# Kernel optimization log

Hardware: AMD Instinct MI355X
Metric: run time of the kernel (lower is better)

## Reference

```python
import jax, jax.numpy as jnp
import numpy as np

T, HID, H, HKV, D = 4096, 2048, 16, 2, 128
EPS = 1e-6


def setup_inputs() -> dict:
    key = jax.random.key(0)
    ks = jax.random.split(key, 5)
    hidden_states = jax.random.normal(ks[0], (T, HID), dtype=jnp.float32)
    # rope angles: build realistic cos/sin from positions and inv-freqs
    inv_freq = 1.0 / (10000.0 ** (jnp.arange(0, D, 2, dtype=jnp.float32) / D))
    ang = jnp.arange(T, dtype=jnp.float32)[:, None] * inv_freq[None, :]  # [T, D/2]
    ang = jnp.concatenate([ang, ang], axis=-1)  # [T, D]
    cos, sin = jnp.cos(ang), jnp.sin(ang)
    w_qkv = jax.random.normal(ks[1], (HID, (2 * H + 2 * HKV) * D), dtype=jnp.float32) * (HID ** -0.5)
    w_o = jax.random.normal(ks[2], (H * D, HID), dtype=jnp.float32) * ((H * D) ** -0.5)
    q_norm_w = jnp.ones((D,), dtype=jnp.float32)
    k_norm_w = jnp.ones((D,), dtype=jnp.float32)
    return {"hidden_states": hidden_states, "cos": cos, "sin": sin,
            "w_qkv": w_qkv, "w_o": w_o, "q_norm_w": q_norm_w, "k_norm_w": k_norm_w}


def _rms_norm(x, w):
    var = jnp.mean(x * x, axis=-1, keepdims=True)
    return x * jax.lax.rsqrt(var + EPS) * w


def _rotate_half(x):
    x1, x2 = x[..., : D // 2], x[..., D // 2:]
    return jnp.concatenate([-x2, x1], axis=-1)


def _rope(x, cos, sin):
    # x: [T, h, D]; cos/sin: [T, D]
    return x * cos[:, None, :] + _rotate_half(x) * sin[:, None, :]


def reference(hidden_states, cos, sin, w_qkv, w_o, q_norm_w, k_norm_w):
    qkv = hidden_states @ w_qkv  # [T, (2H+2HKV)*D]
    q_sz, kv_sz = 2 * H * D, HKV * D
    # packed query+gate: view as [T, H, 2D], first half query, second half gate
    qg = qkv[:, :q_sz].reshape(T, H, 2 * D)
    q, gate = qg[..., :D], qg[..., D:]
    k = qkv[:, q_sz:q_sz + kv_sz].reshape(T, HKV, D)
    v = qkv[:, q_sz + kv_sz:].reshape(T, HKV, D)
    q = _rms_norm(q, q_norm_w)
    k = _rms_norm(k, k_norm_w)
    q = _rope(q, cos, sin)
    k = _rope(k, cos, sin)
    # GQA: expand kv heads to H
    rep = H // HKV
    k = jnp.repeat(k, rep, axis=1)  # [T, H, D]
    v = jnp.repeat(v, rep, axis=1)
    scale = D ** -0.5
    scores = jnp.einsum('thd,shd->hts', q, k) * scale  # [H, T, T]
    causal = jnp.tril(jnp.ones((T, T), dtype=bool))
    scores = jnp.where(causal[None], scores, jnp.finfo(scores.dtype).min)
    probs = jax.nn.softmax(scores, axis=-1)
    attn = jnp.einsum('hts,shd->thd', probs, v)  # [T, H, D]
    out = attn.reshape(T, H * D) * jax.nn.sigmoid(gate.reshape(T, H * D))
    return out @ w_o
```

## Files before the change

kernel.cpp:

```cpp
#include <hip/hip_runtime.h>
#include <hip/hip_bf16.h>
#include <math.h>


namespace {
constexpr int kT   = 4096;
constexpr int kHid = 2048;
constexpr int kH   = 16;
constexpr int kHkv = 2;
constexpr int kD   = 128;
constexpr int kNqkv = (2 * kH + 2 * kHkv) * kD;
constexpr int kQsz  = 2 * kH * kD;
constexpr int kRowU = kNqkv * 2;
constexpr float kEps = 1e-6f;
constexpr float kScale = 0.08838834764831845f;
}

typedef __attribute__((ext_vector_type(8))) short short8;
typedef __attribute__((ext_vector_type(4))) float floatx4;

__device__ inline unsigned short f2bf(float x) {
  unsigned u = __float_as_uint(x);
  u = (u + 0x7fffu + ((u >> 16) & 1u)) >> 16;
  return (unsigned short)u;
}

__device__ inline void gload_lds16(const void* g, void* l) {
  typedef const __attribute__((address_space(1))) unsigned GQ;
  typedef __attribute__((address_space(3))) unsigned LQ;
  __builtin_amdgcn_global_load_lds((GQ*)g, (LQ*)l, 16, 0, 0);
}

__global__ __launch_bounds__(256)
void cvt_bf16(const float* __restrict__ in, unsigned short* __restrict__ out,
              long nelem) {
  long i = ((long)blockIdx.x * 256 + threadIdx.x) * 4;
  if (i >= nelem) return;
  float4 v = *(const float4*)(in + i);
  unsigned long long p = (unsigned long long)f2bf(v.x) |
                         ((unsigned long long)f2bf(v.y) << 16) |
                         ((unsigned long long)f2bf(v.z) << 32) |
                         ((unsigned long long)f2bf(v.w) << 48);
  *(unsigned long long*)(out + i) = p;
}

__global__ __launch_bounds__(256)
void transpose_cvt(const float* __restrict__ in, unsigned short* __restrict__ out,
                   int R, int C) {
  __shared__ float t[32][33];
  const int bx = blockIdx.x * 32;
  const int by = blockIdx.y * 32;
  const int x = threadIdx.x & 31, y = threadIdx.x >> 5;
#pragma unroll
  for (int j = 0; j < 4; ++j)
    t[y * 4 + j][x] = in[(long)(by + y * 4 + j) * C + bx + x];
  __syncthreads();
#pragma unroll
  for (int j = 0; j < 4; ++j)
    out[(long)(bx + y * 4 + j) * R + by + x] = f2bf(t[x][y * 4 + j]);
}

__global__ __launch_bounds__(256)
void vt_transpose(const float* __restrict__ qkv, unsigned short* __restrict__ VtG) {
  __shared__ float t[32][33];
  const int t0 = blockIdx.x * 32;
  const int c0 = blockIdx.y * 32;
  const int x = threadIdx.x & 31, y = threadIdx.x >> 5;
#pragma unroll
  for (int j = 0; j < 4; ++j)
    t[y * 4 + j][x] = qkv[(long)(t0 + y * 4 + j) * kNqkv + 4352 + c0 + x];
  __syncthreads();
#pragma unroll
  for (int j = 0; j < 4; ++j)
    VtG[(long)(c0 + y * 4 + j) * kT + t0 + x] = f2bf(t[x][y * 4 + j]);
}

__global__ __launch_bounds__(256)
void gemm_bf16(const unsigned short* __restrict__ A,
               const unsigned short* __restrict__ Bt, float* __restrict__ C,
               int M, int N, int K) {
  __shared__ __align__(16) unsigned short As[128 * 64];
  __shared__ __align__(16) unsigned short Bs[128 * 64];
  const int tid = threadIdx.x;
  const int lane = tid & 63;
  const int w = tid >> 6;
  const int wr = w >> 1, wc = w & 1;
  const int n = lane & 15;
  const int quad = lane >> 4;
  const long bm = (long)blockIdx.x * 128, bn = (long)blockIdx.y * 128;

  floatx4 acc[4][4];
  floatx4 zero = {0.f, 0.f, 0.f, 0.f};
#pragma unroll
  for (int a = 0; a < 4; ++a)
#pragma unroll
    for (int b = 0; b < 4; ++b) acc[a][b] = zero;

  for (int k0 = 0; k0 < K; k0 += 64) {
    __syncthreads();
#pragma unroll
    for (int it = 0; it < 4; ++it) {
      int ci = it * 256 + tid;
      int r = ci >> 3, c = ci & 7;
      int cg = c ^ (r & 7);
      gload_lds16(A + (bm + r) * (long)K + k0 + cg * 8, As + (it * 256 + w * 64) * 8);
      gload_lds16(Bt + (bn + r) * (long)K + k0 + cg * 8, Bs + (it * 256 + w * 64) * 8);
    }
    __syncthreads();

#pragma unroll
    for (int ks = 0; ks < 2; ++ks) {
      short8 af[4], bf[4];
#pragma unroll
      for (int a = 0; a < 4; ++a) {
        int m = wr * 64 + a * 16 + n;
        af[a] = *(const short8*)(As + m * 64 + ((4 * ks + quad) ^ (m & 7)) * 8);
      }
#pragma unroll
      for (int b = 0; b < 4; ++b) {
        int nn = wc * 64 + b * 16 + n;
        bf[b] = *(const short8*)(Bs + nn * 64 + ((4 * ks + quad) ^ (nn & 7)) * 8);
      }
#pragma unroll
      for (int a = 0; a < 4; ++a)
#pragma unroll
        for (int b = 0; b < 4; ++b)
          acc[a][b] = __builtin_amdgcn_mfma_f32_16x16x32_bf16(af[a], bf[b], acc[a][b], 0, 0, 0);
    }
  }
#pragma unroll
  for (int a = 0; a < 4; ++a)
#pragma unroll
    for (int b = 0; b < 4; ++b)
#pragma unroll
      for (int r = 0; r < 4; ++r)
        C[(bm + wr * 64 + a * 16 + quad * 4 + r) * (long)N + bn + wc * 64 + b * 16 + n] =
            acc[a][b][r];
}

__global__ __launch_bounds__(256)
void norm_rope_cvt(float* qkv, const float* __restrict__ cosb,
                   const float* __restrict__ sinb, const float* __restrict__ qw,
                   const float* __restrict__ kw) {
  unsigned short* qkvu = (unsigned short*)qkv;
  const int lane = threadIdx.x & 63;
  const int wslot = blockIdx.x * 4 + (threadIdx.x >> 6);
  const int nslots = gridDim.x * 4;
  for (int task = wslot; task < kT * 18; task += nslots) {
    const int t = task / 18;
    const int h = task % 18;
    const bool isq = (h < kH);
    const long base = (long)t * kNqkv + (isq ? h * 2 * kD : kQsz + (h - kH) * kD);
    float xlo = qkv[base + lane];
    float xhi = qkv[base + 64 + lane];
    float v = xlo * xlo + xhi * xhi;
#pragma unroll
    for (int off = 1; off < 64; off <<= 1) v += __shfl_xor(v, off, 64);
    float rms = rsqrtf(v * (1.0f / kD) + kEps);
    const float* wv = isq ? qw : kw;
    float nlo = xlo * rms * wv[lane];
    float nhi = xhi * rms * wv[64 + lane];
    float clo = cosb[t * kD + lane], chi = cosb[t * kD + 64 + lane];
    float slo = sinb[t * kD + lane], shi = sinb[t * kD + 64 + lane];
    float rlo = nlo * clo - nhi * slo;
    float rhi = nhi * chi + nlo * shi;
    if (isq) {
      float glo = qkv[base + kD + lane];
      float ghi = qkv[base + kD + 64 + lane];
      qkv[base + kD + lane] = 1.0f / (1.0f + __expf(-glo));
      qkv[base + kD + 64 + lane] = 1.0f / (1.0f + __expf(-ghi));
      qkvu[(long)t * kRowU + 512 * h + lane] = f2bf(rlo);
      qkvu[(long)t * kRowU + 512 * h + 64 + lane] = f2bf(rhi);
    } else {
      qkvu[(long)t * kRowU + 8192 + 256 * (h - kH) + lane] = f2bf(rlo);
      qkvu[(long)t * kRowU + 8192 + 256 * (h - kH) + 64 + lane] = f2bf(rhi);
    }
  }
}

__global__ __launch_bounds__(256)
void flash_attn_mfma(const unsigned short* qkvu, const float* qkvf,
                     const unsigned short* VtG, unsigned short* __restrict__ og) {
  __shared__ __align__(16) unsigned short Ks[64 * 128];
  __shared__ __align__(16) unsigned short Vt[128 * 64];
  __shared__ __align__(16) unsigned short Ps[128 * 64];

  const int tid = threadIdx.x;
  const int lane = tid & 63;
  const int w = tid >> 6;
  const int n = lane & 15;
  const int quad = lane >> 4;
  const int g = blockIdx.x;
  const int h = g & 15;
  const int bm = 31 - (g >> 4);
  const int hk = h >> 3;
  const int q0 = bm * 128;

  short8 qf[2][4];
#pragma unroll
  for (int mt = 0; mt < 2; ++mt) {
    const unsigned short* qrow =
        qkvu + (long)(q0 + 32 * w + 16 * mt + n) * kRowU + 512 * h;
#pragma unroll
    for (int ks = 0; ks < 4; ++ks)
      qf[mt][ks] = *(const short8*)(qrow + 32 * ks + 8 * quad);
  }
  short8 lfrag;
  {
    short o = (n == 0) ? (short)0x3F80 : (short)0;
    lfrag = (short8){o, o, o, o, o, o, o, o};
  }

  floatx4 O[2][8];
  floatx4 Ol[2];
  floatx4 zero = {0.f, 0.f, 0.f, 0.f};
#pragma unroll
  for (int mt = 0; mt < 2; ++mt) {
    Ol[mt] = zero;
#pragma unroll
    for (int dt = 0; dt < 8; ++dt) O[mt][dt] = zero;
  }

  const int kn_end = 2 * bm + 1;
  for (int kn = 0; kn <= kn_end; ++kn) {
    __syncthreads();
#pragma unroll
    for (int it = 0; it < 4; ++it) {
      int pc = (w * 4 + it) * 64 + lane;
      int r = pc >> 4, c = pc & 15;
      int lc = c ^ (r & 15);
      gload_lds16(qkvu + (long)(kn * 64 + r) * kRowU + 8192 + 256 * hk + 8 * lc,
                  Ks + (w * 4 + it) * 512);
    }
#pragma unroll
    for (int it = 0; it < 4; ++it) {
      int pc = (w * 4 + it) * 64 + lane;
      int d = pc >> 3, c = pc & 7;
      int lc = c ^ (d & 7);
      gload_lds16(VtG + (long)hk * (128 * kT) + (long)d * kT + kn * 64 + 8 * lc,
                  Vt + (w * 4 + it) * 512);
    }
    __syncthreads();

    floatx4 S[2][4];
#pragma unroll
    for (int mt = 0; mt < 2; ++mt)
#pragma unroll
      for (int ct = 0; ct < 4; ++ct) S[mt][ct] = zero;
#pragma unroll
    for (int ks = 0; ks < 4; ++ks) {
#pragma unroll
      for (int ct = 0; ct < 4; ++ct) {
        int row = 16 * ct + n;
        short8 kf = *(const short8*)(Ks + row * 128 + ((4 * ks + quad) ^ n) * 8);
        S[0][ct] = __builtin_amdgcn_mfma_f32_16x16x32_bf16(qf[0][ks], kf, S[0][ct], 0, 0, 0);
        S[1][ct] = __builtin_amdgcn_mfma_f32_16x16x32_bf16(qf[1][ks], kf, S[1][ct], 0, 0, 0);
      }
    }

    const bool needmask = (kn >= 2 * bm);
    const int jbase = (kn - 2 * bm) * 64;
    const int hi = n >> 3, lo = n & 7;
#pragma unroll
    for (int mt = 0; mt < 2; ++mt) {
#pragma unroll
      for (int r = 0; r < 4; ++r) {
        int prow = 32 * w + 16 * mt + quad * 4 + r;
        float p0 = __expf(S[mt][0][r] * kScale);
        float p1 = __expf(S[mt][1][r] * kScale);
        float p2 = __expf(S[mt][2][r] * kScale);
        float p3 = __expf(S[mt][3][r] * kScale);
        if (needmask) {
          if (jbase + n > prow) p0 = 0.f;
          if (jbase + 16 + n > prow) p1 = 0.f;
          if (jbase + 32 + n > prow) p2 = 0.f;
          if (jbase + 48 + n > prow) p3 = 0.f;
        }
        int sw = prow & 7;
        Ps[prow * 64 + (((0 + hi) ^ sw) << 3) + lo] = f2bf(p0);
        Ps[prow * 64 + (((2 + hi) ^ sw) << 3) + lo] = f2bf(p1);
        Ps[prow * 64 + (((4 + hi) ^ sw) << 3) + lo] = f2bf(p2);
        Ps[prow * 64 + (((6 + hi) ^ sw) << 3) + lo] = f2bf(p3);
      }
    }
    __asm__ volatile("s_waitcnt lgkmcnt(0)" ::: "memory");

#pragma unroll
    for (int ks = 0; ks < 2; ++ks) {
      int r0 = 32 * w + n, r1 = 32 * w + 16 + n;
      short8 pf0 = *(const short8*)(Ps + r0 * 64 + (((4 * ks + quad) ^ (r0 & 7)) << 3));
      short8 pf1 = *(const short8*)(Ps + r1 * 64 + (((4 * ks + quad) ^ (r1 & 7)) << 3));
      Ol[0] = __builtin_amdgcn_mfma_f32_16x16x32_bf16(pf0, lfrag, Ol[0], 0, 0, 0);
      Ol[1] = __builtin_amdgcn_mfma_f32_16x16x32_bf16(pf1, lfrag, Ol[1], 0, 0, 0);
#pragma unroll
      for (int dt = 0; dt < 8; ++dt) {
        int d = 16 * dt + n;
        short8 vf = *(const short8*)(Vt + d * 64 + (((4 * ks + quad) ^ (d & 7)) << 3));
        O[0][dt] = __builtin_amdgcn_mfma_f32_16x16x32_bf16(pf0, vf, O[0][dt], 0, 0, 0);
        O[1][dt] = __builtin_amdgcn_mfma_f32_16x16x32_bf16(pf1, vf, O[1][dt], 0, 0, 0);
      }
    }
  }

#pragma unroll
  for (int mt = 0; mt < 2; ++mt) {
#pragma unroll
    for (int r = 0; r < 4; ++r) {
      float l = __shfl(Ol[mt][r], quad << 4, 64);
      float inv = 1.0f / l;
      int row = q0 + 32 * w + 16 * mt + quad * 4 + r;
#pragma unroll
      for (int dt = 0; dt < 8; ++dt) {
        int col = 16 * dt + n;
        float gte = qkvf[(long)row * kNqkv + 256 * h + 128 + col];
        og[(long)row * kHid + 128 * h + col] = f2bf(O[mt][dt][r] * inv * gte);
      }
    }
  }
}

extern "C" void kernel_launch(void* const* d_in, const int* in_sizes, int n_in,
                              void* d_out, int out_size, void* d_ws, size_t ws_size,
                              hipStream_t stream) {
  (void)in_sizes; (void)n_in; (void)out_size; (void)ws_size;
  const float* hs   = (const float*)d_in[0];
  const float* cosb = (const float*)d_in[1];
  const float* sinb = (const float*)d_in[2];
  const float* wqkv = (const float*)d_in[3];
  const float* wo   = (const float*)d_in[4];
  const float* qw   = (const float*)d_in[5];
  const float* kw   = (const float*)d_in[6];
  float* out = (float*)d_out;

  char* ws = (char*)d_ws;
  float* qkv = (float*)ws;
  unsigned short* hsb = (unsigned short*)(ws + 75497472);
  unsigned short* og  = hsb;
  unsigned short* wt  = (unsigned short*)(ws + 92274688);
  unsigned short* VtG = wt;

  cvt_bf16<<<dim3(8192), 256, 0, stream>>>(hs, hsb, (long)kT * kHid);
  transpose_cvt<<<dim3(kNqkv / 32, kHid / 32), 256, 0, stream>>>(wqkv, wt, kHid, kNqkv);
  gemm_bf16<<<dim3(kT / 128, kNqkv / 128), 256, 0, stream>>>(hsb, wt, qkv, kT, kNqkv, kHid);
  vt_transpose<<<dim3(kT / 32, 8), 256, 0, stream>>>(qkv, VtG);
  norm_rope_cvt<<<dim3(2304), 256, 0, stream>>>(qkv, cosb, sinb, qw, kw);
  flash_attn_mfma<<<dim3(kT / 128 * kH), 256, 0, stream>>>((const unsigned short*)qkv, qkv, VtG, og);
  transpose_cvt<<<dim3(kHid / 32, kHid / 32), 256, 0, stream>>>(wo, wt, kHid, kHid);
  gemm_bf16<<<dim3(kT / 128, kHid / 128), 256, 0, stream>>>(og, wt, out, kT, kHid, kHid);
}
```

Baseline: 483.3 us.

## Split causal attention key range across two blocks and combine partials

```diff
diff --git a/kernel.cpp b/kernel.cpp
--- a/kernel.cpp
+++ b/kernel.cpp
@@ -23,6 +23,10 @@
   unsigned u = __float_as_uint(x);
   u = (u + 0x7fffu + ((u >> 16) & 1u)) >> 16;
   return (unsigned short)u;
+}
+
+__device__ inline float bf2f(unsigned short u) {
+  return __uint_as_float((unsigned)u << 16);
 }
 
 __device__ inline void gload_lds16(const void* g, void* l) {
@@ -179,8 +183,8 @@
 }
 
 __global__ __launch_bounds__(256)
-void flash_attn_mfma(const unsigned short* qkvu, const float* qkvf,
-                     const unsigned short* VtG, unsigned short* __restrict__ og) {
+void flash_attn_mfma(const unsigned short* qkvu, float* qkvf,
+                     const unsigned short* VtG, unsigned short* __restrict__ ogp) {
   __shared__ __align__(16) unsigned short Ks[64 * 128];
   __shared__ __align__(16) unsigned short Vt[128 * 64];
   __shared__ __align__(16) unsigned short Ps[128 * 64];
@@ -192,7 +196,9 @@
   const int quad = lane >> 4;
   const int g = blockIdx.x;
   const int h = g & 15;
-  const int bm = 31 - (g >> 4);
+  const int gi = g >> 4;
+  const int bm = 31 - (gi >> 1);
+  const int half = gi & 1;
   const int hk = h >> 3;
   const int q0 = bm * 128;
 
@@ -221,8 +227,9 @@
     for (int dt = 0; dt < 8; ++dt) O[mt][dt] = zero;
   }
 
-  const int kn_end = 2 * bm + 1;
-  for (int kn = 0; kn <= kn_end; ++kn) {
+  const int kn0 = half ? (bm + 1) : 0;
+  const int kn1 = half ? (2 * bm + 1) : bm;
+  for (int kn = kn0; kn <= kn1; ++kn) {
     __syncthreads();
 #pragma unroll
     for (int it = 0; it < 4; ++it) {
@@ -302,21 +309,43 @@
     }
   }
 
+  unsigned short* obuf = half ? (unsigned short*)qkvf : ogp;
 #pragma unroll
   for (int mt = 0; mt < 2; ++mt) {
 #pragma unroll
     for (int r = 0; r < 4; ++r) {
-      float l = __shfl(Ol[mt][r], quad << 4, 64);
-      float inv = 1.0f / l;
       int row = q0 + 32 * w + 16 * mt + quad * 4 + r;
-#pragma unroll
-      for (int dt = 0; dt < 8; ++dt) {
-        int col = 16 * dt + n;
-        float gte = qkvf[(long)row * kNqkv + 256 * h + 128 + col];
-        og[(long)row * kHid + 128 * h + col] = f2bf(O[mt][dt][r] * inv * gte);
-      }
-    }
-  }
+      if (n == 0)
+        qkvf[(long)row * kNqkv + (half ? 4368 : 4352) + h] = Ol[mt][r];
+      long base = half ? ((long)row * kRowU + 512 * h + 128)
+                       : ((long)row * kHid + 128 * h);
+#pragma unroll
+      for (int dt = 0; dt < 8; ++dt)
+        obuf[base + 16 * dt + n] = f2bf(O[mt][dt][r]);
+    }
+  }
+}
+
+__global__ __launch_bounds__(256)
+void attn_combine(float* qkvf, unsigned short* og) {
+  const unsigned short* qkvu = (const unsigned short*)qkvf;
+  const int tid = threadIdx.x;
+  const int row = blockIdx.x * 16 + (tid >> 4);
+  const int d0 = (tid & 15) * 8;
+  const int t = row >> 4, h = row & 15;
+  short8 oa = *(const short8*)(og + (long)t * kHid + 128 * h + d0);
+  short8 ob = *(const short8*)(qkvu + (long)t * kRowU + 512 * h + 128 + d0);
+  float la = qkvf[(long)t * kNqkv + 4352 + h];
+  float lb = qkvf[(long)t * kNqkv + 4368 + h];
+  float inv = 1.0f / (la + lb);
+  const float* gate = qkvf + (long)t * kNqkv + 256 * h + 128 + d0;
+  short8 res;
+#pragma unroll
+  for (int j = 0; j < 8; ++j) {
+    float o = bf2f((unsigned short)oa[j]) + bf2f((unsigned short)ob[j]);
+    res[j] = (short)f2bf(o * inv * gate[j]);
+  }
+  *(short8*)(og + (long)t * kHid + 128 * h + d0) = res;
 }
 
 extern "C" void kernel_launch(void* const* d_in, const int* in_sizes, int n_in,
@@ -344,7 +373,8 @@
   gemm_bf16<<<dim3(kT / 128, kNqkv / 128), 256, 0, stream>>>(hsb, wt, qkv, kT, kNqkv, kHid);
   vt_transpose<<<dim3(kT / 32, 8), 256, 0, stream>>>(qkv, VtG);
   norm_rope_cvt<<<dim3(2304), 256, 0, stream>>>(qkv, cosb, sinb, qw, kw);
-  flash_attn_mfma<<<dim3(kT / 128 * kH), 256, 0, stream>>>((const unsigned short*)qkv, qkv, VtG, og);
+  flash_attn_mfma<<<dim3(kT / 128 * kH * 2), 256, 0, stream>>>((const unsigned short*)qkv, qkv, VtG, og);
+  attn_combine<<<dim3(kT * kH / 16), 256, 0, stream>>>(qkv, og);
   transpose_cvt<<<dim3(kHid / 32, kHid / 32), 256, 0, stream>>>(wo, wt, kHid, kHid);
-  gemm_bf16<<<dim3(kT / 128, kHid / 128), 256, 0, stream>>>(og, wt, out, kT, kHid, kHid);
-}
+  gemm_bf16<<<dim3(kT / 128, kHid / 128), 256, 0, stream>>>(og, wt, out, kHid == 2048 ? kT : kT, kHid, kHid);
+}
```

Result: no change. 488.8 us (+1.1%).

## Use 256x256-tile double-buffered bf16 GEMM with 512 threads for QKV projection

Applied to the files above, without the earlier changes.

```diff
diff --git a/kernel.cpp b/kernel.cpp
--- a/kernel.cpp
+++ b/kernel.cpp
@@ -73,6 +73,132 @@
 #pragma unroll
   for (int j = 0; j < 4; ++j)
     VtG[(long)(c0 + y * 4 + j) * kT + t0 + x] = f2bf(t[x][y * 4 + j]);
+}
+
+__global__ __launch_bounds__(512)
+void gemm256(const unsigned short* __restrict__ A,
+             const unsigned short* __restrict__ Bt, float* __restrict__ C,
+             int M, int N, int K) {
+  __shared__ __align__(16) unsigned short As[2][2][8192];
+  __shared__ __align__(16) unsigned short Bs[2][2][8192];
+  const int tid = threadIdx.x;
+  const int lane = tid & 63;
+  const int w = tid >> 6;
+  const int wm = w >> 2, wn = w & 3;
+  const int n16 = lane & 15, quad = lane >> 4;
+  const long bm = (long)blockIdx.x * 256, bn = (long)blockIdx.y * 256;
+  const int NT = K >> 6;
+
+  floatx4 acc[8][4];
+  floatx4 zero = {0.f, 0.f, 0.f, 0.f};
+#pragma unroll
+  for (int mf = 0; mf < 8; ++mf)
+#pragma unroll
+    for (int nf = 0; nf < 4; ++nf) acc[mf][nf] = zero;
+
+  auto stageA = [&](int p, int kh, int kt) {
+#pragma unroll
+    for (int it = 0; it < 2; ++it) {
+      int ci = it * 512 + tid;
+      int r = ci & 255, cpos = ci >> 8;
+      gload_lds16(A + (bm + r) * (long)K + kt * 64 + kh * 32 + cpos * 8,
+                  &As[p][kh][(it * 512 + w * 64) * 8]);
+    }
+  };
+  auto stageB = [&](int p, int kh, int kt) {
+#pragma unroll
+    for (int it = 0; it < 2; ++it) {
+      int ci = it * 512 + tid;
+      int r = ci & 255, cpos = ci >> 8;
+      gload_lds16(Bt + (bn + r) * (long)K + kt * 64 + kh * 32 + cpos * 8,
+                  &Bs[p][kh][(it * 512 + w * 64) * 8]);
+    }
+  };
+
+  stageA(0, 0, 0); stageB(0, 0, 0); stageA(0, 1, 0); stageB(0, 1, 0);
+  __asm__ volatile("s_waitcnt vmcnt(0)" ::: "memory");
+  __builtin_amdgcn_s_barrier();
+  __builtin_amdgcn_sched_barrier(0);
+
+  for (int t = 0; t < NT; ++t) {
+    const int p = t & 1, ps = p ^ 1;
+    const bool pre = (t + 1 < NT);
+    short8 af[8], bf[2];
+
+    if (pre) stageA(ps, 0, t + 1);
+#pragma unroll
+    for (int mf = 0; mf < 8; ++mf)
+      af[mf] = *(const short8*)(&As[p][0][(quad * 256 + wm * 128 + mf * 16 + n16) * 8]);
+#pragma unroll
+    for (int nf = 0; nf < 2; ++nf)
+      bf[nf] = *(const short8*)(&Bs[p][0][(quad * 256 + wn * 64 + nf * 16 + n16) * 8]);
+    __builtin_amdgcn_s_setprio(1);
+#pragma unroll
+    for (int mf = 0; mf < 8; ++mf)
+#pragma unroll
+      for (int nf = 0; nf < 2; ++nf)
+        acc[mf][nf] = __builtin_amdgcn_mfma_f32_16x16x32_bf16(af[mf], bf[nf], acc[mf][nf], 0, 0, 0);
+    __builtin_amdgcn_s_setprio(0);
+
+    if (pre) stageB(ps, 0, t + 1);
+#pragma unroll
+    for (int nf = 0; nf < 2; ++nf)
+      bf[nf] = *(const short8*)(&Bs[p][0][(quad * 256 + wn * 64 + (nf + 2) * 16 + n16) * 8]);
+    __builtin_amdgcn_s_setprio(1);
+#pragma unroll
+    for (int mf = 0; mf < 8; ++mf)
+#pragma unroll
+      for (int nf = 0; nf < 2; ++nf)
+        acc[mf][nf + 2] = __builtin_amdgcn_mfma_f32_16x16x32_bf16(af[mf], bf[nf], acc[mf][nf + 2], 0, 0, 0);
+    __builtin_amdgcn_s_setprio(0);
+
+    if (pre) { __asm__ volatile("s_waitcnt vmcnt(4)" ::: "memory"); }
+    else     { __asm__ volatile("s_waitcnt vmcnt(0)" ::: "memory"); }
+    __builtin_amdgcn_s_barrier();
+    __builtin_amdgcn_sched_barrier(0);
+
+    if (pre) stageA(ps, 1, t + 1);
+#pragma unroll
+    for (int mf = 0; mf < 8; ++mf)
+      af[mf] = *(const short8*)(&As[p][1][(quad * 256 + wm * 128 + mf * 16 + n16) * 8]);
+#pragma unroll
+    for (int nf = 0; nf < 2; ++nf)
+      bf[nf] = *(const short8*)(&Bs[p][1][(quad * 256 + wn * 64 + nf * 16 + n16) * 8]);
+    __builtin_amdgcn_s_setprio(1);
+#pragma unroll
+    for (int mf = 0; mf < 8; ++mf)
+#pragma unroll
+      for (int nf = 0; nf < 2; ++nf)
+        acc[mf][nf] = __builtin_amdgcn_mfma_f32_16x16x32_bf16(af[mf], bf[nf], acc[mf][nf], 0, 0, 0);
+    __builtin_amdgcn_s_setprio(0);
+
+    if (pre) stageB(ps, 1, t + 1);
+#pragma unroll
+    for (int nf = 0; nf < 2; ++nf)
+      bf[nf] = *(const short8*)(&Bs[p][1][(quad * 256 + wn * 64 + (nf + 2) * 16 + n16) * 8]);
+    __builtin_amdgcn_s_setprio(1);
+#pragma unroll
+    for (int mf = 0; mf < 8; ++mf)
+#pragma unroll
+      for (int nf = 0; nf < 2; ++nf)
+        acc[mf][nf + 2] = __builtin_amdgcn_mfma_f32_16x16x32_bf16(af[mf], bf[nf], acc[mf][nf + 2], 0, 0, 0);
+    __builtin_amdgcn_s_setprio(0);
+
+    if (pre) {
+      __asm__ volatile("s_waitcnt vmcnt(4)" ::: "memory");
+      __builtin_amdgcn_s_barrier();
+      __builtin_amdgcn_sched_barrier(0);
+    }
+  }
+
+#pragma unroll
+  for (int mf = 0; mf < 8; ++mf)
+#pragma unroll
+    for (int nf = 0; nf < 4; ++nf)
+#pragma unroll
+      for (int r = 0; r < 4; ++r)
+        C[(bm + wm * 128 + mf * 16 + quad * 4 + r) * (long)N + bn + wn * 64 + nf * 16 + n16] =
+            acc[mf][nf][r];
 }
 
 __global__ __launch_bounds__(256)
@@ -341,7 +467,7 @@
 
   cvt_bf16<<<dim3(8192), 256, 0, stream>>>(hs, hsb, (long)kT * kHid);
   transpose_cvt<<<dim3(kNqkv / 32, kHid / 32), 256, 0, stream>>>(wqkv, wt, kHid, kNqkv);
-  gemm_bf16<<<dim3(kT / 128, kNqkv / 128), 256, 0, stream>>>(hsb, wt, qkv, kT, kNqkv, kHid);
+  gemm256<<<dim3(kT / 256, kNqkv / 256), 512, 0, stream>>>(hsb, wt, qkv, kT, kNqkv, kHid);
   vt_transpose<<<dim3(kT / 32, 8), 256, 0, stream>>>(qkv, VtG);
   norm_rope_cvt<<<dim3(2304), 256, 0, stream>>>(qkv, cosb, sinb, qw, kw);
   flash_attn_mfma<<<dim3(kT / 128 * kH), 256, 0, stream>>>((const unsigned short*)qkv, qkv, VtG, og);
```

Result: slower. 569.6 us (+17.9%).
